# Kernel tuning notes

Hardware: AMD Instinct MI355X
Metric: run time of the kernel (lower is better)

## Reference

```python
import jax, jax.numpy as jnp
import numpy as np

NEG_SLOPE_ATT = 0.2   # GATConv leaky_relu slope on attention logits
NEG_SLOPE_ACT = 0.01  # F.leaky_relu default between layers


def _gat_layer(x, src, dst, W, a_src, a_dst, b, concat):
    """PyG GATConv (eval mode, self-loops already appended to src/dst).
    x: [N, F_in]; W: [F_in, H*C]; a_src/a_dst: [H, C]; b: [H*C] or [C].
    """
    N = x.shape[0]
    H, C = a_src.shape
    h = (x @ W).reshape(N, H, C)                      # [N,H,C]
    e_src = jnp.einsum('nhc,hc->nh', h, a_src)        # [N,H]
    e_dst = jnp.einsum('nhc,hc->nh', h, a_dst)        # [N,H]
    alpha = jax.nn.leaky_relu(e_src[src] + e_dst[dst], NEG_SLOPE_ATT)  # [E,H]
    # segment softmax over destination neighborhoods
    m = jax.ops.segment_max(alpha, dst, num_segments=N)               # [N,H]
    ex = jnp.exp(alpha - m[dst])
    denom = jax.ops.segment_sum(ex, dst, num_segments=N)              # [N,H]
    coef = ex / denom[dst]                                            # [E,H]
    out = jax.ops.segment_sum(h[src] * coef[:, :, None], dst, num_segments=N)  # [N,H,C]
    out = out.reshape(N, H * C) if concat else out.mean(axis=1)
    return out + b


def setup_inputs() -> dict:
    key = jax.random.key(0)
    ks = jax.random.split(key, 12)
    N, E, F_IN, HID, HEADS, OUT = 100000, 1600000, 128, 32, 4, 64
    x = jax.random.normal(ks[0], (N, F_IN), dtype=jnp.float32)
    edge_index = jax.random.randint(ks[1], (2, E), 0, N, dtype=jnp.int32)
    s1 = 1.0 / np.sqrt(F_IN)
    s2 = 1.0 / np.sqrt(HEADS * HID)
    return {
        'x': x,
        'edge_index': edge_index,
        'W1': jax.random.normal(ks[2], (F_IN, HEADS * HID), dtype=jnp.float32) * s1,
        'att_src1': jax.random.normal(ks[3], (HEADS, HID), dtype=jnp.float32) * s2,
        'att_dst1': jax.random.normal(ks[4], (HEADS, HID), dtype=jnp.float32) * s2,
        'b1': jnp.zeros((HEADS * HID,), dtype=jnp.float32),
        'W2': jax.random.normal(ks[5], (HEADS * HID, OUT), dtype=jnp.float32) * s2,
        'att_src2': jax.random.normal(ks[6], (1, OUT), dtype=jnp.float32) * (1.0 / np.sqrt(OUT)),
        'att_dst2': jax.random.normal(ks[7], (1, OUT), dtype=jnp.float32) * (1.0 / np.sqrt(OUT)),
        'b2': jnp.zeros((OUT,), dtype=jnp.float32),
    }


def reference(x, edge_index, W1, att_src1, att_dst1, b1, W2, att_src2, att_dst2, b2):
    N = x.shape[0]
    loops = jnp.arange(N, dtype=edge_index.dtype)
    src = jnp.concatenate([edge_index[0], loops])
    dst = jnp.concatenate([edge_index[1], loops])
    # dropout layers are identity in eval mode
    h = _gat_layer(x, src, dst, W1, att_src1, att_dst1, b1, concat=True)
    h = jax.nn.leaky_relu(h, NEG_SLOPE_ACT)
    out = _gat_layer(h, src, dst, W2, att_src2, att_dst2, b2, concat=False)
    return out
```

## Files before the change

### kernel.cpp

```cpp
#include <hip/hip_runtime.h>
#include <hip/hip_bf16.h>

typedef short bf16x8 __attribute__((ext_vector_type(8)));
typedef float f32x4 __attribute__((ext_vector_type(4)));

__device__ __forceinline__ unsigned pack_bf16x2(float lo, float hi) {
    unsigned a = __builtin_bit_cast(unsigned, lo);
    unsigned b = __builtin_bit_cast(unsigned, hi);
    a += 0x7fffu + ((a >> 16) & 1u);
    b += 0x7fffu + ((b >> 16) & 1u);
    return (a >> 16) | (b & 0xffff0000u);
}
__device__ __forceinline__ unsigned short bf16r(float f) {
    unsigned a = __builtin_bit_cast(unsigned, f);
    a += 0x7fffu + ((a >> 16) & 1u);
    return (unsigned short)(a >> 16);
}
__device__ __forceinline__ float bf_lo(unsigned u) {
    return __builtin_bit_cast(float, u << 16);
}
__device__ __forceinline__ float bf_hi(unsigned u) {
    return __builtin_bit_cast(float, u & 0xffff0000u);
}

__global__ void prep_kernel(const float* __restrict__ W1, const float* __restrict__ W2,
                            unsigned* __restrict__ Wb1, unsigned* __restrict__ Wb2,
                            int* __restrict__ deg, int N) {
    const int t = blockIdx.x * 256 + threadIdx.x;
    if (t < 2048) {
        const int lane = t & 63, kt = (t >> 6) & 3, ct = t >> 8;
        const int col = ct * 16 + (lane & 15);
        const int kb = 8 * (lane >> 4) + 32 * kt;
        uint4 u;
        u.x = pack_bf16x2(W1[(size_t)(kb + 0) * 128 + col], W1[(size_t)(kb + 1) * 128 + col]);
        u.y = pack_bf16x2(W1[(size_t)(kb + 2) * 128 + col], W1[(size_t)(kb + 3) * 128 + col]);
        u.z = pack_bf16x2(W1[(size_t)(kb + 4) * 128 + col], W1[(size_t)(kb + 5) * 128 + col]);
        u.w = pack_bf16x2(W1[(size_t)(kb + 6) * 128 + col], W1[(size_t)(kb + 7) * 128 + col]);
        *(uint4*)&Wb1[t * 4] = u;
    } else if (t < 3072) {
        const int s = t - 2048;
        const int lane = s & 63, kt = (s >> 6) & 3, ct = s >> 8;
        const int col = ct * 16 + (lane & 15);
        const int kb = 8 * (lane >> 4) + 32 * kt;
        uint4 u;
        u.x = pack_bf16x2(W2[(size_t)(kb + 0) * 64 + col], W2[(size_t)(kb + 1) * 64 + col]);
        u.y = pack_bf16x2(W2[(size_t)(kb + 2) * 64 + col], W2[(size_t)(kb + 3) * 64 + col]);
        u.z = pack_bf16x2(W2[(size_t)(kb + 4) * 64 + col], W2[(size_t)(kb + 5) * 64 + col]);
        u.w = pack_bf16x2(W2[(size_t)(kb + 6) * 64 + col], W2[(size_t)(kb + 7) * 64 + col]);
        *(uint4*)&Wb2[s * 4] = u;
    }
    for (int i = t; i < N; i += gridDim.x * 256) deg[i] = 0;
}

__global__ __launch_bounds__(256) void gemm1_kernel(const float* __restrict__ x,
                                                    const unsigned* __restrict__ Wb1,
                                                    const float* __restrict__ asrc,
                                                    const float* __restrict__ adst,
                                                    unsigned short* __restrict__ h1,
                                                    float* __restrict__ es,
                                                    float* __restrict__ ed,
                                                    int N) {
    const int wid = threadIdx.x >> 6, lane = threadIdx.x & 63;
    const int row0 = (blockIdx.x * 4 + wid) * 16;
    if (row0 >= N) return;
    const int g = lane >> 4, l16 = lane & 15;
    const int mrow = min(row0 + l16, N - 1);

    bf16x8 afrag[4];
#pragma unroll
    for (int kt = 0; kt < 4; ++kt) {
        const float4 v0 = *(const float4*)&x[(size_t)mrow * 128 + g * 8 + kt * 32];
        const float4 v1 = *(const float4*)&x[(size_t)mrow * 128 + g * 8 + kt * 32 + 4];
        uint4 u;
        u.x = pack_bf16x2(v0.x, v0.y);
        u.y = pack_bf16x2(v0.z, v0.w);
        u.z = pack_bf16x2(v1.x, v1.y);
        u.w = pack_bf16x2(v1.z, v1.w);
        afrag[kt] = __builtin_bit_cast(bf16x8, u);
    }
    float psh[4][4] = {};
    float pdh[4][4] = {};
#pragma unroll
    for (int ct = 0; ct < 8; ++ct) {
        f32x4 acc = {0.f, 0.f, 0.f, 0.f};
#pragma unroll
        for (int kt = 0; kt < 4; ++kt) {
            const bf16x8 b = __builtin_bit_cast(bf16x8, *(const uint4*)&Wb1[((ct * 4 + kt) * 64 + lane) * 4]);
            acc = __builtin_amdgcn_mfma_f32_16x16x32_bf16(afrag[kt], b, acc, 0, 0, 0);
        }
        const int col = ct * 16 + l16;
        const float as_ = asrc[col], ad_ = adst[col];
        const int hh = ct >> 1;
#pragma unroll
        for (int r = 0; r < 4; ++r) {
            psh[hh][r] = fmaf(acc[r], as_, psh[hh][r]);
            pdh[hh][r] = fmaf(acc[r], ad_, pdh[hh][r]);
        }
#pragma unroll
        for (int r = 0; r < 4; ++r) {
            const int row = row0 + g * 4 + r;
            if (row < N) h1[(size_t)row * 128 + col] = bf16r(acc[r]);
        }
    }
#pragma unroll
    for (int hh = 0; hh < 4; ++hh)
#pragma unroll
        for (int r = 0; r < 4; ++r) {
#pragma unroll
            for (int off = 1; off <= 8; off <<= 1) {
                psh[hh][r] += __shfl_xor(psh[hh][r], off);
                pdh[hh][r] += __shfl_xor(pdh[hh][r], off);
            }
        }
    if (l16 == 0) {
#pragma unroll
        for (int r = 0; r < 4; ++r) {
            const int row = row0 + g * 4 + r;
            if (row < N) {
#pragma unroll
                for (int hh = 0; hh < 4; ++hh) {
                    es[row * 4 + hh] = psh[hh][r];
                    ed[row * 4 + hh] = pdh[hh][r];
                }
            }
        }
    }
}

__global__ __launch_bounds__(256) void gemm2_kernel(const unsigned* __restrict__ x2p,
                                                    const unsigned* __restrict__ Wb2,
                                                    const float* __restrict__ asrc,
                                                    const float* __restrict__ adst,
                                                    unsigned short* __restrict__ h2,
                                                    float* __restrict__ es,
                                                    float* __restrict__ ed,
                                                    int N) {
    const int wid = threadIdx.x >> 6, lane = threadIdx.x & 63;
    const int row0 = (blockIdx.x * 4 + wid) * 16;
    if (row0 >= N) return;
    const int g = lane >> 4, l16 = lane & 15;
    const int mrow = min(row0 + l16, N - 1);

    bf16x8 afrag[4];
#pragma unroll
    for (int kt = 0; kt < 4; ++kt)
        afrag[kt] = __builtin_bit_cast(bf16x8, *(const uint4*)&x2p[(size_t)mrow * 64 + g * 4 + kt * 16]);
    float ps[4] = {}, pd[4] = {};
#pragma unroll
    for (int ct = 0; ct < 4; ++ct) {
        f32x4 acc = {0.f, 0.f, 0.f, 0.f};
#pragma unroll
        for (int kt = 0; kt < 4; ++kt) {
            const bf16x8 b = __builtin_bit_cast(bf16x8, *(const uint4*)&Wb2[((ct * 4 + kt) * 64 + lane) * 4]);
            acc = __builtin_amdgcn_mfma_f32_16x16x32_bf16(afrag[kt], b, acc, 0, 0, 0);
        }
        const int col = ct * 16 + l16;
        const float as_ = asrc[col], ad_ = adst[col];
#pragma unroll
        for (int r = 0; r < 4; ++r) {
            ps[r] = fmaf(acc[r], as_, ps[r]);
            pd[r] = fmaf(acc[r], ad_, pd[r]);
        }
#pragma unroll
        for (int r = 0; r < 4; ++r) {
            const int row = row0 + g * 4 + r;
            if (row < N) h2[(size_t)row * 64 + col] = bf16r(acc[r]);
        }
    }
#pragma unroll
    for (int r = 0; r < 4; ++r) {
#pragma unroll
        for (int off = 1; off <= 8; off <<= 1) {
            ps[r] += __shfl_xor(ps[r], off);
            pd[r] += __shfl_xor(pd[r], off);
        }
    }
    if (l16 == 0) {
#pragma unroll
        for (int r = 0; r < 4; ++r) {
            const int row = row0 + g * 4 + r;
            if (row < N) { es[row] = ps[r]; ed[row] = pd[r]; }
        }
    }
}

__global__ __launch_bounds__(256) void rank_count_kernel(const int* __restrict__ ei, int E,
                                                         int* __restrict__ deg,
                                                         int* __restrict__ rank) {
    const int stride = gridDim.x * 256;
    int e = blockIdx.x * 256 + threadIdx.x;
    for (; e + 7 * stride < E; e += 8 * stride) {
        int d[8], r[8];
#pragma unroll
        for (int i = 0; i < 8; ++i) d[i] = ei[E + e + i * stride];
#pragma unroll
        for (int i = 0; i < 8; ++i) r[i] = atomicAdd(&deg[d[i]], 1);
#pragma unroll
        for (int i = 0; i < 8; ++i) rank[e + i * stride] = r[i];
    }
    for (; e < E; e += stride)
        rank[e] = atomicAdd(&deg[ei[E + e]], 1);
}

__global__ __launch_bounds__(256) void scan_p1_kernel(const int* __restrict__ deg,
                                                      int* __restrict__ excl,
                                                      int* __restrict__ bsum, int N) {
    __shared__ int lds[256];
    const int tid = threadIdx.x;
    const int base = blockIdx.x * 2048;
    const int idx0 = base + tid * 8;
    int v[8];
    int s = 0;
#pragma unroll
    for (int i = 0; i < 8; ++i) {
        v[i] = (idx0 + i < N) ? deg[idx0 + i] + 1 : 0;
        s += v[i];
    }
    lds[tid] = s;
    __syncthreads();
    for (int off = 1; off < 256; off <<= 1) {
        int t = (tid >= off) ? lds[tid - off] : 0;
        __syncthreads();
        lds[tid] += t;
        __syncthreads();
    }
    const int texcl = lds[tid] - s;
    if (tid == 255) bsum[blockIdx.x] = lds[255];
    int run = texcl;
#pragma unroll
    for (int i = 0; i < 8; ++i) {
        if (idx0 + i < N) excl[idx0 + i] = run;
        run += v[i];
    }
}

__global__ void scan_p2_kernel(int* __restrict__ bsum, int nchunks) {
    const int lane = threadIdx.x;
    int v = (lane < nchunks) ? bsum[lane] : 0;
    const int orig = v;
#pragma unroll
    for (int off = 1; off < 64; off <<= 1) {
        int t = __shfl_up(v, off);
        if (lane >= off) v += t;
    }
    if (lane < nchunks) bsum[lane] = v - orig;
}

__global__ void scan_p3_kernel(const int* __restrict__ excl, const int* __restrict__ bsum,
                               int* __restrict__ rowstart, int N, int Etot) {
    const int i = blockIdx.x * 256 + threadIdx.x;
    if (i < N) rowstart[i] = excl[i] + bsum[i >> 11];
    if (i == 0) rowstart[N] = Etot;
}

__global__ void csr_fill_kernel(const int* __restrict__ ei, int E, int N,
                                const int* __restrict__ rowstart,
                                const int* __restrict__ rank,
                                int* __restrict__ csr_src) {
    const int e = blockIdx.x * 256 + threadIdx.x;
    if (e < E) {
        const int d = ei[E + e];
        csr_src[rowstart[d] + rank[e]] = ei[e];
    } else if (e < E + N) {
        const int d = e - E;
        csr_src[rowstart[d + 1] - 1] = d;
    }
}

__global__ __launch_bounds__(256) void aggregate1_kernel(const unsigned* __restrict__ h1p,
                                                         const float* __restrict__ es,
                                                         const float* __restrict__ ed,
                                                         const int* __restrict__ rowstart,
                                                         const int* __restrict__ csr_src,
                                                         const float* __restrict__ b,
                                                         unsigned* __restrict__ x2p, int N) {
    const int lane = threadIdx.x & 63;
    const int w = (blockIdx.x * 256 + threadIdx.x) >> 6;
    const int l16 = lane & 15;
    const int n = w * 4 + (lane >> 4);
    const int hh = l16 >> 2;
    const bool valid = n < N;
    const int nc = valid ? n : N - 1;
    const int beg = rowstart[nc];
    const int deg = valid ? rowstart[nc + 1] - beg : 0;
    const float edv = ed[nc * 4 + hh];

    int dmax = deg;
    dmax = max(dmax, __shfl_xor(dmax, 16));
    dmax = max(dmax, __shfl_xor(dmax, 32));

    float acc0 = 0.f, acc1 = 0.f, acc2 = 0.f, acc3 = 0.f;
    float acc4 = 0.f, acc5 = 0.f, acc6 = 0.f, acc7 = 0.f;
    float den = 0.f;
    for (int j = 0; j < dmax; j += 4) {
        const bool va = j < deg, vb = j + 1 < deg, vc = j + 2 < deg, vd = j + 3 < deg;
        const int pa_ = va ? beg + j : 0;
        const int pb_ = vb ? beg + j + 1 : 0;
        const int pc_ = vc ? beg + j + 2 : 0;
        const int pd_ = vd ? beg + j + 3 : 0;
        const int sa = csr_src[pa_];
        const int sb = csr_src[pb_];
        const int sc = csr_src[pc_];
        const int sd = csr_src[pd_];
        const uint4 ua = *(const uint4*)&h1p[(size_t)sa * 64 + l16 * 4];
        const uint4 ub = *(const uint4*)&h1p[(size_t)sb * 64 + l16 * 4];
        const uint4 uc = *(const uint4*)&h1p[(size_t)sc * 64 + l16 * 4];
        const uint4 ud = *(const uint4*)&h1p[(size_t)sd * 64 + l16 * 4];
        const float xa = es[sa * 4 + hh] + edv;
        const float xb = es[sb * 4 + hh] + edv;
        const float xc = es[sc * 4 + hh] + edv;
        const float xd = es[sd * 4 + hh] + edv;
        float qa = __expf(fmaxf(xa, 0.2f * xa));
        float qb = __expf(fmaxf(xb, 0.2f * xb));
        float qc = __expf(fmaxf(xc, 0.2f * xc));
        float qd = __expf(fmaxf(xd, 0.2f * xd));
        qa = va ? qa : 0.f;
        qb = vb ? qb : 0.f;
        qc = vc ? qc : 0.f;
        qd = vd ? qd : 0.f;
        den += (qa + qb) + (qc + qd);
        acc0 = fmaf(qa, bf_lo(ua.x), fmaf(qb, bf_lo(ub.x), fmaf(qc, bf_lo(uc.x), fmaf(qd, bf_lo(ud.x), acc0))));
        acc1 = fmaf(qa, bf_hi(ua.x), fmaf(qb, bf_hi(ub.x), fmaf(qc, bf_hi(uc.x), fmaf(qd, bf_hi(ud.x), acc1))));
        acc2 = fmaf(qa, bf_lo(ua.y), fmaf(qb, bf_lo(ub.y), fmaf(qc, bf_lo(uc.y), fmaf(qd, bf_lo(ud.y), acc2))));
        acc3 = fmaf(qa, bf_hi(ua.y), fmaf(qb, bf_hi(ub.y), fmaf(qc, bf_hi(uc.y), fmaf(qd, bf_hi(ud.y), acc3))));
        acc4 = fmaf(qa, bf_lo(ua.z), fmaf(qb, bf_lo(ub.z), fmaf(qc, bf_lo(uc.z), fmaf(qd, bf_lo(ud.z), acc4))));
        acc5 = fmaf(qa, bf_hi(ua.z), fmaf(qb, bf_hi(ub.z), fmaf(qc, bf_hi(uc.z), fmaf(qd, bf_hi(ud.z), acc5))));
        acc6 = fmaf(qa, bf_lo(ua.w), fmaf(qb, bf_lo(ub.w), fmaf(qc, bf_lo(uc.w), fmaf(qd, bf_lo(ud.w), acc6))));
        acc7 = fmaf(qa, bf_hi(ua.w), fmaf(qb, bf_hi(ub.w), fmaf(qc, bf_hi(uc.w), fmaf(qd, bf_hi(ud.w), acc7))));
    }
    if (valid) {
        const float inv = __builtin_amdgcn_rcpf(den);
        const float4 ba = *(const float4*)&b[l16 * 8];
        const float4 bb = *(const float4*)&b[l16 * 8 + 4];
        float o0 = fmaf(acc0, inv, ba.x); o0 = fmaxf(o0, 0.01f * o0);
        float o1 = fmaf(acc1, inv, ba.y); o1 = fmaxf(o1, 0.01f * o1);
        float o2 = fmaf(acc2, inv, ba.z); o2 = fmaxf(o2, 0.01f * o2);
        float o3 = fmaf(acc3, inv, ba.w); o3 = fmaxf(o3, 0.01f * o3);
        float o4 = fmaf(acc4, inv, bb.x); o4 = fmaxf(o4, 0.01f * o4);
        float o5 = fmaf(acc5, inv, bb.y); o5 = fmaxf(o5, 0.01f * o5);
        float o6 = fmaf(acc6, inv, bb.z); o6 = fmaxf(o6, 0.01f * o6);
        float o7 = fmaf(acc7, inv, bb.w); o7 = fmaxf(o7, 0.01f * o7);
        uint4 o;
        o.x = pack_bf16x2(o0, o1);
        o.y = pack_bf16x2(o2, o3);
        o.z = pack_bf16x2(o4, o5);
        o.w = pack_bf16x2(o6, o7);
        *(uint4*)&x2p[(size_t)n * 64 + l16 * 4] = o;
    }
}

__global__ __launch_bounds__(256) void aggregate2_kernel(const unsigned* __restrict__ h2p,
                                                         const float* __restrict__ es,
                                                         const float* __restrict__ ed,
                                                         const int* __restrict__ rowstart,
                                                         const int* __restrict__ csr_src,
                                                         const float* __restrict__ b,
                                                         float* __restrict__ out, int N) {
    const int lane = threadIdx.x & 63;
    const int w = (blockIdx.x * 256 + threadIdx.x) >> 6;
    const int l16 = lane & 15;
    const int n = w * 4 + (lane >> 4);
    const bool valid = n < N;
    const int nc = valid ? n : N - 1;
    const int beg = rowstart[nc];
    const int deg = valid ? rowstart[nc + 1] - beg : 0;
    const float edv = ed[nc];

    int dmax = deg;
    dmax = max(dmax, __shfl_xor(dmax, 16));
    dmax = max(dmax, __shfl_xor(dmax, 32));

    float acc0 = 0.f, acc1 = 0.f, acc2 = 0.f, acc3 = 0.f;
    float den = 0.f;
    for (int j = 0; j < dmax; j += 4) {
        const bool va = j < deg, vb = j + 1 < deg, vc = j + 2 < deg, vd = j + 3 < deg;
        const int pa_ = va ? beg + j : 0;
        const int pb_ = vb ? beg + j + 1 : 0;
        const int pc_ = vc ? beg + j + 2 : 0;
        const int pd_ = vd ? beg + j + 3 : 0;
        const int sa = csr_src[pa_];
        const int sb = csr_src[pb_];
        const int sc = csr_src[pc_];
        const int sd = csr_src[pd_];
        const uint2 ua = *(const uint2*)&h2p[(size_t)sa * 32 + l16 * 2];
        const uint2 ub = *(const uint2*)&h2p[(size_t)sb * 32 + l16 * 2];
        const uint2 uc = *(const uint2*)&h2p[(size_t)sc * 32 + l16 * 2];
        const uint2 ud = *(const uint2*)&h2p[(size_t)sd * 32 + l16 * 2];
        const float xa = es[sa] + edv;
        const float xb = es[sb] + edv;
        const float xc = es[sc] + edv;
        const float xd = es[sd] + edv;
        float qa = __expf(fmaxf(xa, 0.2f * xa));
        float qb = __expf(fmaxf(xb, 0.2f * xb));
        float qc = __expf(fmaxf(xc, 0.2f * xc));
        float qd = __expf(fmaxf(xd, 0.2f * xd));
        qa = va ? qa : 0.f;
        qb = vb ? qb : 0.f;
        qc = vc ? qc : 0.f;
        qd = vd ? qd : 0.f;
        den += (qa + qb) + (qc + qd);
        acc0 = fmaf(qa, bf_lo(ua.x), fmaf(qb, bf_lo(ub.x), fmaf(qc, bf_lo(uc.x), fmaf(qd, bf_lo(ud.x), acc0))));
        acc1 = fmaf(qa, bf_hi(ua.x), fmaf(qb, bf_hi(ub.x), fmaf(qc, bf_hi(uc.x), fmaf(qd, bf_hi(ud.x), acc1))));
        acc2 = fmaf(qa, bf_lo(ua.y), fmaf(qb, bf_lo(ub.y), fmaf(qc, bf_lo(uc.y), fmaf(qd, bf_lo(ud.y), acc2))));
        acc3 = fmaf(qa, bf_hi(ua.y), fmaf(qb, bf_hi(ub.y), fmaf(qc, bf_hi(uc.y), fmaf(qd, bf_hi(ud.y), acc3))));
    }
    if (valid) {
        const float inv = __builtin_amdgcn_rcpf(den);
        const float4 bv = *(const float4*)&b[l16 * 4];
        float4 o;
        o.x = fmaf(acc0, inv, bv.x);
        o.y = fmaf(acc1, inv, bv.y);
        o.z = fmaf(acc2, inv, bv.z);
        o.w = fmaf(acc3, inv, bv.w);
        *(float4*)&out[(size_t)n * 64 + l16 * 4] = o;
    }
}

extern "C" void kernel_launch(void* const* d_in, const int* in_sizes, int n_in,
                              void* d_out, int out_size, void* d_ws, size_t ws_size,
                              hipStream_t stream) {
    const float* x     = (const float*)d_in[0];
    const int*   ei    = (const int*)d_in[1];
    const float* W1    = (const float*)d_in[2];
    const float* asrc1 = (const float*)d_in[3];
    const float* adst1 = (const float*)d_in[4];
    const float* b1    = (const float*)d_in[5];
    const float* W2    = (const float*)d_in[6];
    const float* asrc2 = (const float*)d_in[7];
    const float* adst2 = (const float*)d_in[8];
    const float* b2    = (const float*)d_in[9];
    float* out = (float*)d_out;

    const int N = in_sizes[0] / 128;
    const int E = in_sizes[1] / 2;
    const int Etot = E + N;

    char* p = (char*)d_ws;
    auto alloc = [&](size_t bytes) {
        char* q = p;
        p += (bytes + 255) & ~size_t(255);
        return q;
    };
    unsigned short* h1 = (unsigned short*)alloc((size_t)N * 128 * 2);
    unsigned* x2p      = (unsigned*)alloc((size_t)N * 64 * 4);
    unsigned short* h2 = (unsigned short*)alloc((size_t)N * 64 * 2);
    float* es1      = (float*)alloc((size_t)N * 4 * 4);
    float* ed1      = (float*)alloc((size_t)N * 4 * 4);
    float* es2      = (float*)alloc((size_t)N * 4);
    float* ed2      = (float*)alloc((size_t)N * 4);
    int*   deg      = (int*)alloc((size_t)N * 4);
    int*   excl     = (int*)alloc((size_t)N * 4);
    int*   bsum     = (int*)alloc(1024);
    int*   rowstart = (int*)alloc((size_t)(N + 1) * 4);
    int*   rank     = (int*)alloc((size_t)E * 4);
    int*   csr_src  = (int*)alloc((size_t)Etot * 4);
    unsigned* Wb1   = (unsigned*)alloc(2048 * 16);
    unsigned* Wb2   = (unsigned*)alloc(1024 * 16);

    const int nblk16 = (N + 63) / 64;
    const int nwb4 = (N + 15) / 16;
    const int nchunks = (N + 2047) / 2048;

    prep_kernel<<<64, 256, 0, stream>>>(W1, W2, Wb1, Wb2, deg, N);

    gemm1_kernel<<<nblk16, 256, 0, stream>>>(x, Wb1, asrc1, adst1, h1, es1, ed1, N);

    rank_count_kernel<<<512, 256, 0, stream>>>(ei, E, deg, rank);
    scan_p1_kernel<<<nchunks, 256, 0, stream>>>(deg, excl, bsum, N);
    scan_p2_kernel<<<1, 64, 0, stream>>>(bsum, nchunks);
    scan_p3_kernel<<<(N + 255) / 256, 256, 0, stream>>>(excl, bsum, rowstart, N, Etot);
    csr_fill_kernel<<<(Etot + 255) / 256, 256, 0, stream>>>(ei, E, N, rowstart, rank, csr_src);

    aggregate1_kernel<<<nwb4, 256, 0, stream>>>((const unsigned*)h1, es1, ed1,
                                                rowstart, csr_src, b1, x2p, N);

    gemm2_kernel<<<nblk16, 256, 0, stream>>>(x2p, Wb2, asrc2, adst2, h2, es2, ed2, N);
    aggregate2_kernel<<<nwb4, 256, 0, stream>>>((const unsigned*)h2, es2, ed2,
                                                rowstart, csr_src, b2, out, N);
}
```

Measured before the change: 258.2 us.

## Pad degree counters to 64-byte stride and give each thread contiguous edges

Degree counters move from a dense int array to one counter per 64-byte slot, so that random atomics from different edges no longer contend on the same cache line. The rank-count kernel also switches from a grid-stride loop to one contiguous 8-edge chunk per thread, with the grid sized to E. The padding makes the counter array 16x larger, which raises cache footprint and makes the zeroing and the scan read strided, poorly coalesced memory.

```diff
diff --git a/kernel.cpp b/kernel.cpp
--- a/kernel.cpp
+++ b/kernel.cpp
@@ -25,7 +25,7 @@
 
 __global__ void prep_kernel(const float* __restrict__ W1, const float* __restrict__ W2,
                             unsigned* __restrict__ Wb1, unsigned* __restrict__ Wb2,
-                            int* __restrict__ deg, int N) {
+                            int* __restrict__ deg_p, int N) {
     const int t = blockIdx.x * 256 + threadIdx.x;
     if (t < 2048) {
         const int lane = t & 63, kt = (t >> 6) & 3, ct = t >> 8;
@@ -49,7 +49,7 @@
         u.w = pack_bf16x2(W2[(size_t)(kb + 6) * 64 + col], W2[(size_t)(kb + 7) * 64 + col]);
         *(uint4*)&Wb2[s * 4] = u;
     }
-    for (int i = t; i < N; i += gridDim.x * 256) deg[i] = 0;
+    for (int i = t; i < N; i += gridDim.x * 256) deg_p[(size_t)i * 16] = 0;
 }
 
 __global__ __launch_bounds__(256) void gemm1_kernel(const float* __restrict__ x,
@@ -185,24 +185,25 @@
 }
 
 __global__ __launch_bounds__(256) void rank_count_kernel(const int* __restrict__ ei, int E,
-                                                         int* __restrict__ deg,
+                                                         int* __restrict__ deg_p,
                                                          int* __restrict__ rank) {
-    const int stride = gridDim.x * 256;
-    int e = blockIdx.x * 256 + threadIdx.x;
-    for (; e + 7 * stride < E; e += 8 * stride) {
+    const int base = (blockIdx.x * 256 + threadIdx.x) * 8;
+    if (base >= E) return;
+    if (base + 8 <= E) {
         int d[8], r[8];
 #pragma unroll
-        for (int i = 0; i < 8; ++i) d[i] = ei[E + e + i * stride];
-#pragma unroll
-        for (int i = 0; i < 8; ++i) r[i] = atomicAdd(&deg[d[i]], 1);
-#pragma unroll
-        for (int i = 0; i < 8; ++i) rank[e + i * stride] = r[i];
-    }
-    for (; e < E; e += stride)
-        rank[e] = atomicAdd(&deg[ei[E + e]], 1);
-}
-
-__global__ __launch_bounds__(256) void scan_p1_kernel(const int* __restrict__ deg,
+        for (int i = 0; i < 8; ++i) d[i] = ei[E + base + i];
+#pragma unroll
+        for (int i = 0; i < 8; ++i) r[i] = atomicAdd(&deg_p[(size_t)d[i] * 16], 1);
+#pragma unroll
+        for (int i = 0; i < 8; ++i) rank[base + i] = r[i];
+    } else {
+        for (int e = base; e < E; ++e)
+            rank[e] = atomicAdd(&deg_p[(size_t)ei[E + e] * 16], 1);
+    }
+}
+
+__global__ __launch_bounds__(256) void scan_p1_kernel(const int* __restrict__ deg_p,
                                                       int* __restrict__ excl,
                                                       int* __restrict__ bsum, int N) {
     __shared__ int lds[256];
@@ -213,7 +214,7 @@
     int s = 0;
 #pragma unroll
     for (int i = 0; i < 8; ++i) {
-        v[i] = (idx0 + i < N) ? deg[idx0 + i] + 1 : 0;
+        v[i] = (idx0 + i < N) ? deg_p[(size_t)(idx0 + i) * 16] + 1 : 0;
         s += v[i];
     }
     lds[tid] = s;
@@ -448,7 +449,7 @@
     float* ed1      = (float*)alloc((size_t)N * 4 * 4);
     float* es2      = (float*)alloc((size_t)N * 4);
     float* ed2      = (float*)alloc((size_t)N * 4);
-    int*   deg      = (int*)alloc((size_t)N * 4);
+    int*   deg_p    = (int*)alloc((size_t)N * 64);
     int*   excl     = (int*)alloc((size_t)N * 4);
     int*   bsum     = (int*)alloc(1024);
     int*   rowstart = (int*)alloc((size_t)(N + 1) * 4);
@@ -459,14 +460,15 @@
 
     const int nblk16 = (N + 63) / 64;
     const int nwb4 = (N + 15) / 16;
+    const int nrank = (E + 2047) / 2048;
     const int nchunks = (N + 2047) / 2048;
 
-    prep_kernel<<<64, 256, 0, stream>>>(W1, W2, Wb1, Wb2, deg, N);
+    prep_kernel<<<64, 256, 0, stream>>>(W1, W2, Wb1, Wb2, deg_p, N);
 
     gemm1_kernel<<<nblk16, 256, 0, stream>>>(x, Wb1, asrc1, adst1, h1, es1, ed1, N);
 
-    rank_count_kernel<<<512, 256, 0, stream>>>(ei, E, deg, rank);
-    scan_p1_kernel<<<nchunks, 256, 0, stream>>>(deg, excl, bsum, N);
+    rank_count_kernel<<<nrank, 256, 0, stream>>>(ei, E, deg_p, rank);
+    scan_p1_kernel<<<nchunks, 256, 0, stream>>>(deg_p, excl, bsum, N);
     scan_p2_kernel<<<1, 64, 0, stream>>>(bsum, nchunks);
     scan_p3_kernel<<<(N + 255) / 256, 256, 0, stream>>>(excl, bsum, rowstart, N, Etot);
     csr_fill_kernel<<<(Etot + 255) / 256, 256, 0, stream>>>(ei, E, N, rowstart, rank, csr_src);
```

New measurement: 259.1 us. No clear change (+0.4%).

## Build CSR via two-level bucket sort instead of global atomic rank counting

Applied to the files above, without the earlier changes.

Replaces the per-edge global atomic degree/rank counting, three-pass scan and random scatter with a two-level bucket sort. Edges are first histogrammed and scattered into 256-node destination buckets using LDS atomics, then each bucket is sorted into CSR in a single block with a local scan. This is meant to cut contended global atomics and random global writes. The cost is two extra Etot-sized temporary arrays and an extra pass over edge data. Within-row edge order becomes nondeterministic, which only changes floating-point summation order.

```diff
diff --git a/kernel.cpp b/kernel.cpp
--- a/kernel.cpp
+++ b/kernel.cpp
@@ -25,7 +25,7 @@
 
 __global__ void prep_kernel(const float* __restrict__ W1, const float* __restrict__ W2,
                             unsigned* __restrict__ Wb1, unsigned* __restrict__ Wb2,
-                            int* __restrict__ deg, int N) {
+                            int* __restrict__ gcount) {
     const int t = blockIdx.x * 256 + threadIdx.x;
     if (t < 2048) {
         const int lane = t & 63, kt = (t >> 6) & 3, ct = t >> 8;
@@ -49,7 +49,7 @@
         u.w = pack_bf16x2(W2[(size_t)(kb + 6) * 64 + col], W2[(size_t)(kb + 7) * 64 + col]);
         *(uint4*)&Wb2[s * 4] = u;
     }
-    for (int i = t; i < N; i += gridDim.x * 256) deg[i] = 0;
+    if (t < 512) gcount[t] = 0;
 }
 
 __global__ __launch_bounds__(256) void gemm1_kernel(const float* __restrict__ x,
@@ -184,86 +184,120 @@
     }
 }
 
-__global__ __launch_bounds__(256) void rank_count_kernel(const int* __restrict__ ei, int E,
-                                                         int* __restrict__ deg,
-                                                         int* __restrict__ rank) {
-    const int stride = gridDim.x * 256;
-    int e = blockIdx.x * 256 + threadIdx.x;
-    for (; e + 7 * stride < E; e += 8 * stride) {
-        int d[8], r[8];
-#pragma unroll
-        for (int i = 0; i < 8; ++i) d[i] = ei[E + e + i * stride];
-#pragma unroll
-        for (int i = 0; i < 8; ++i) r[i] = atomicAdd(&deg[d[i]], 1);
-#pragma unroll
-        for (int i = 0; i < 8; ++i) rank[e + i * stride] = r[i];
-    }
-    for (; e < E; e += stride)
-        rank[e] = atomicAdd(&deg[ei[E + e]], 1);
-}
-
-__global__ __launch_bounds__(256) void scan_p1_kernel(const int* __restrict__ deg,
-                                                      int* __restrict__ excl,
-                                                      int* __restrict__ bsum, int N) {
-    __shared__ int lds[256];
-    const int tid = threadIdx.x;
-    const int base = blockIdx.x * 2048;
-    const int idx0 = base + tid * 8;
-    int v[8];
-    int s = 0;
-#pragma unroll
-    for (int i = 0; i < 8; ++i) {
-        v[i] = (idx0 + i < N) ? deg[idx0 + i] + 1 : 0;
-        s += v[i];
-    }
-    lds[tid] = s;
+
+__global__ __launch_bounds__(256) void bucket_hist_kernel(const int* __restrict__ ei, int E,
+                                                          int* __restrict__ gcount) {
+    __shared__ int h[512];
+    for (int i = threadIdx.x; i < 512; i += 256) h[i] = 0;
+    __syncthreads();
+    for (int e = blockIdx.x * 256 + threadIdx.x; e < E; e += gridDim.x * 256)
+        atomicAdd(&h[ei[E + e] >> 8], 1);
+    __syncthreads();
+    for (int i = threadIdx.x; i < 512; i += 256)
+        if (h[i]) atomicAdd(&gcount[i], h[i]);
+}
+
+__global__ __launch_bounds__(256) void bucket_scan_kernel(const int* __restrict__ gcount,
+                                                          int* __restrict__ bucket_base,
+                                                          int* __restrict__ cursor,
+                                                          int* __restrict__ rowstart,
+                                                          int N, int NB, int Etot) {
+    __shared__ int pairs[256];
+    const int t = threadIdx.x;
+    const int b0 = 2 * t, b1 = 2 * t + 1;
+    int v0 = 0, v1 = 0;
+    if (b0 < NB) v0 = gcount[b0] + min(256, N - b0 * 256);
+    if (b1 < NB) v1 = gcount[b1] + min(256, N - b1 * 256);
+    const int s = v0 + v1;
+    pairs[t] = s;
     __syncthreads();
     for (int off = 1; off < 256; off <<= 1) {
-        int t = (tid >= off) ? lds[tid - off] : 0;
+        int tv = (t >= off) ? pairs[t - off] : 0;
         __syncthreads();
-        lds[tid] += t;
+        pairs[t] += tv;
         __syncthreads();
     }
-    const int texcl = lds[tid] - s;
-    if (tid == 255) bsum[blockIdx.x] = lds[255];
-    int run = texcl;
-#pragma unroll
-    for (int i = 0; i < 8; ++i) {
-        if (idx0 + i < N) excl[idx0 + i] = run;
-        run += v[i];
-    }
-}
-
-__global__ void scan_p2_kernel(int* __restrict__ bsum, int nchunks) {
-    const int lane = threadIdx.x;
-    int v = (lane < nchunks) ? bsum[lane] : 0;
-    const int orig = v;
-#pragma unroll
-    for (int off = 1; off < 64; off <<= 1) {
-        int t = __shfl_up(v, off);
-        if (lane >= off) v += t;
-    }
-    if (lane < nchunks) bsum[lane] = v - orig;
-}
-
-__global__ void scan_p3_kernel(const int* __restrict__ excl, const int* __restrict__ bsum,
-                               int* __restrict__ rowstart, int N, int Etot) {
-    const int i = blockIdx.x * 256 + threadIdx.x;
-    if (i < N) rowstart[i] = excl[i] + bsum[i >> 11];
-    if (i == 0) rowstart[N] = Etot;
-}
-
-__global__ void csr_fill_kernel(const int* __restrict__ ei, int E, int N,
-                                const int* __restrict__ rowstart,
-                                const int* __restrict__ rank,
-                                int* __restrict__ csr_src) {
-    const int e = blockIdx.x * 256 + threadIdx.x;
-    if (e < E) {
-        const int d = ei[E + e];
-        csr_src[rowstart[d] + rank[e]] = ei[e];
-    } else if (e < E + N) {
-        const int d = e - E;
-        csr_src[rowstart[d + 1] - 1] = d;
+    const int base = pairs[t] - s;
+    if (b0 < NB) bucket_base[b0] = base;
+    if (b1 < NB) bucket_base[b1] = base + v0;
+    if (t == 255) {
+        bucket_base[NB] = pairs[255];
+        rowstart[N] = Etot;
+    }
+    cursor[b0] = 0;
+    cursor[b1] = 0;
+}
+
+__global__ __launch_bounds__(256) void bucket_scatter_kernel(const int* __restrict__ ei,
+                                                             int E, int Etot,
+                                                             const int* __restrict__ bucket_base,
+                                                             int* __restrict__ cursor,
+                                                             int* __restrict__ tmp_dst,
+                                                             int* __restrict__ tmp_src) {
+    __shared__ int lh[512];
+    __shared__ int gb[512];
+    for (int i = threadIdx.x; i < 512; i += 256) lh[i] = 0;
+    __syncthreads();
+    const int base = blockIdx.x * 4096;
+    int d[16], s[16], lr[16];
+#pragma unroll
+    for (int k = 0; k < 16; ++k) {
+        const int e = base + k * 256 + threadIdx.x;
+        if (e < E) { s[k] = ei[e]; d[k] = ei[E + e]; }
+        else if (e < Etot) { d[k] = e - E; s[k] = e - E; }
+        else { d[k] = -1; s[k] = 0; }
+        lr[k] = (d[k] >= 0) ? atomicAdd(&lh[d[k] >> 8], 1) : 0;
+    }
+    __syncthreads();
+    for (int b = threadIdx.x; b < 512; b += 256)
+        gb[b] = lh[b] ? atomicAdd(&cursor[b], lh[b]) : 0;
+    __syncthreads();
+#pragma unroll
+    for (int k = 0; k < 16; ++k) {
+        if (d[k] >= 0) {
+            const int b = d[k] >> 8;
+            const int slot = bucket_base[b] + gb[b] + lr[k];
+            tmp_dst[slot] = d[k];
+            tmp_src[slot] = s[k];
+        }
+    }
+}
+
+__global__ __launch_bounds__(256) void bucket_build_kernel(const int* __restrict__ bucket_base,
+                                                           const int* __restrict__ tmp_dst,
+                                                           const int* __restrict__ tmp_src,
+                                                           int* __restrict__ rowstart,
+                                                           int* __restrict__ csr_src,
+                                                           int N) {
+    __shared__ int cnt[256];
+    __shared__ int sc[256];
+    __shared__ int cur[256];
+    const int b = blockIdx.x;
+    const int beg = bucket_base[b], end = bucket_base[b + 1];
+    const int t = threadIdx.x;
+    cnt[t] = 0;
+    __syncthreads();
+    for (int i = beg + t; i < end; i += 256)
+        atomicAdd(&cnt[tmp_dst[i] & 255], 1);
+    __syncthreads();
+    const int v = cnt[t];
+    sc[t] = v;
+    __syncthreads();
+    for (int off = 1; off < 256; off <<= 1) {
+        int tv = (t >= off) ? sc[t - off] : 0;
+        __syncthreads();
+        sc[t] += tv;
+        __syncthreads();
+    }
+    const int excl = sc[t] - v;
+    const int d_out = b * 256 + t;
+    if (d_out < N) rowstart[d_out] = beg + excl;
+    cur[t] = excl;
+    __syncthreads();
+    for (int i = beg + t; i < end; i += 256) {
+        const int dd = tmp_dst[i];
+        const int idx = atomicAdd(&cur[dd & 255], 1);
+        csr_src[beg + idx] = tmp_src[i];
     }
 }
 
@@ -434,6 +468,7 @@
     const int N = in_sizes[0] / 128;
     const int E = in_sizes[1] / 2;
     const int Etot = E + N;
+    const int NB = (N + 255) >> 8;
 
     char* p = (char*)d_ws;
     auto alloc = [&](size_t bytes) {
@@ -448,28 +483,30 @@
     float* ed1      = (float*)alloc((size_t)N * 4 * 4);
     float* es2      = (float*)alloc((size_t)N * 4);
     float* ed2      = (float*)alloc((size_t)N * 4);
-    int*   deg      = (int*)alloc((size_t)N * 4);
-    int*   excl     = (int*)alloc((size_t)N * 4);
-    int*   bsum     = (int*)alloc(1024);
+    int*   gcount   = (int*)alloc(512 * 4);
+    int*   bucket_base = (int*)alloc(513 * 4);
+    int*   cursor   = (int*)alloc(512 * 4);
     int*   rowstart = (int*)alloc((size_t)(N + 1) * 4);
-    int*   rank     = (int*)alloc((size_t)E * 4);
+    int*   tmp_dst  = (int*)alloc((size_t)Etot * 4);
+    int*   tmp_src  = (int*)alloc((size_t)Etot * 4);
     int*   csr_src  = (int*)alloc((size_t)Etot * 4);
     unsigned* Wb1   = (unsigned*)alloc(2048 * 16);
     unsigned* Wb2   = (unsigned*)alloc(1024 * 16);
 
     const int nblk16 = (N + 63) / 64;
     const int nwb4 = (N + 15) / 16;
-    const int nchunks = (N + 2047) / 2048;
-
-    prep_kernel<<<64, 256, 0, stream>>>(W1, W2, Wb1, Wb2, deg, N);
+    const int nscat = (Etot + 4095) / 4096;
+
+    prep_kernel<<<12, 256, 0, stream>>>(W1, W2, Wb1, Wb2, gcount);
 
     gemm1_kernel<<<nblk16, 256, 0, stream>>>(x, Wb1, asrc1, adst1, h1, es1, ed1, N);
 
-    rank_count_kernel<<<512, 256, 0, stream>>>(ei, E, deg, rank);
-    scan_p1_kernel<<<nchunks, 256, 0, stream>>>(deg, excl, bsum, N);
-    scan_p2_kernel<<<1, 64, 0, stream>>>(bsum, nchunks);
-    scan_p3_kernel<<<(N + 255) / 256, 256, 0, stream>>>(excl, bsum, rowstart, N, Etot);
-    csr_fill_kernel<<<(Etot + 255) / 256, 256, 0, stream>>>(ei, E, N, rowstart, rank, csr_src);
+    bucket_hist_kernel<<<512, 256, 0, stream>>>(ei, E, gcount);
+    bucket_scan_kernel<<<1, 256, 0, stream>>>(gcount, bucket_base, cursor, rowstart, N, NB, Etot);
+    bucket_scatter_kernel<<<nscat, 256, 0, stream>>>(ei, E, Etot, bucket_base, cursor,
+                                                     tmp_dst, tmp_src);
+    bucket_build_kernel<<<NB, 256, 0, stream>>>(bucket_base, tmp_dst, tmp_src,
+                                                rowstart, csr_src, N);
 
     aggregate1_kernel<<<nwb4, 256, 0, stream>>>((const unsigned*)h1, es1, ed1,
                                                 rowstart, csr_src, b1, x2p, N);
```

Result: faster. 228.0 us (-11.7%).
